# Performance work log

Hardware: AMD Instinct MI355X
Metric: run time of the kernel (lower is better)

## Reference

```python
import jax, jax.numpy as jnp
import numpy as np

N, E = 50000, 800000
NF, EF, S = 128, 64, 128

def _lin(key, fan_in, fan_out):
    k1, k2 = jax.random.split(key)
    lim = 1.0 / np.sqrt(fan_in)
    W = jax.random.uniform(k1, (fan_in, fan_out), jnp.float32, -lim, lim)
    b = jax.random.uniform(k2, (fan_out,), jnp.float32, -lim, lim)
    return W, b

def setup_inputs() -> dict:
    key = jax.random.key(0)
    ks = jax.random.split(key, 12)
    x = jax.random.normal(ks[0], (N, NF), jnp.float32)
    edge_index = jax.random.randint(ks[1], (2, E), 0, N, jnp.int64)
    edge_attr = jax.random.normal(ks[2], (E, EF), jnp.float32)
    Wn, bn = _lin(ks[3], NF, S)
    We, be = _lin(ks[4], EF, S)
    Wzc, bzc = _lin(ks[5], S, S)   # GCNConv weight/bias (z gate)
    Wzl, bzl = _lin(ks[6], 2 * S, S)
    Wrc, brc = _lin(ks[7], S, S)
    Wrl, brl = _lin(ks[8], 2 * S, S)
    Whc, bhc = _lin(ks[9], S, S)
    Whl, bhl = _lin(ks[10], 2 * S, S)
    Wout, bout = _lin(ks[11], 3 * S, 1)
    return dict(x=x, edge_index=edge_index, edge_attr=edge_attr,
                Wn=Wn, bn=bn, We=We, be=be,
                Wzc=Wzc, bzc=bzc, Wzl=Wzl, bzl=bzl,
                Wrc=Wrc, brc=brc, Wrl=Wrl, brl=brl,
                Whc=Whc, bhc=bhc, Whl=Whl, bhl=bhl,
                Wout=Wout, bout=bout)

def reference(x, edge_index, edge_attr, Wn, bn, We, be,
              Wzc, bzc, Wzl, bzl, Wrc, brc, Wrl, brl,
              Whc, bhc, Whl, bhl, Wout, bout):
    n = x.shape[0]
    src, dst = edge_index[0], edge_index[1]
    xe = jax.nn.relu(x @ Wn + bn)                      # [N,S]
    ea = jax.nn.relu(edge_attr @ We + be)              # [E,S]
    # GCNConv normalization with self-loops (shared across the 3 gates)
    loop = jnp.arange(n)
    s2 = jnp.concatenate([src, loop])
    d2 = jnp.concatenate([dst, loop])
    deg = jax.ops.segment_sum(jnp.ones(s2.shape[0], xe.dtype), d2, n)
    dinv = jax.lax.rsqrt(deg)                          # deg >= 1 (self loops)
    norm = (dinv[s2] * dinv[d2])[:, None]              # [E+N,1]
    def gcn(W, b):
        xw = xe @ W
        return jax.ops.segment_sum(xw[s2] * norm, d2, n) + b
    H = jnp.zeros_like(xe)
    Z = jax.nn.sigmoid(jnp.concatenate([gcn(Wzc, bzc), H], 1) @ Wzl + bzl)
    R = jax.nn.sigmoid(jnp.concatenate([gcn(Wrc, brc), H], 1) @ Wrl + brl)
    Ht = jnp.tanh(jnp.concatenate([gcn(Whc, bhc), H * R], 1) @ Whl + bhl)
    H = Z * H + (1.0 - Z) * Ht                          # [N,S]
    edge_h = jnp.concatenate([H[src], H[dst], ea], axis=1)  # [E,3S]
    return edge_h @ Wout + bout                         # [E,1]
```

## Files before the change

### kernel.cpp

```cpp
#include <hip/hip_runtime.h>
#include <hip/hip_bf16.h>
#include <math.h>

#define NN 50000
#define EE 800000

typedef __bf16 bf16x8 __attribute__((ext_vector_type(8)));
typedef float f32x4 __attribute__((ext_vector_type(4)));
typedef unsigned int u32x4 __attribute__((ext_vector_type(4)));

__global__ void k_deg_wprep(const int* __restrict__ ei, int* __restrict__ deg,
                            const float* __restrict__ Wzc, const float* __restrict__ bzc,
                            const float* __restrict__ Wzl, const float* __restrict__ bzl,
                            const float* __restrict__ Whc, const float* __restrict__ bhc,
                            const float* __restrict__ Whl, const float* __restrict__ bhl,
                            float* __restrict__ Wcat, float* __restrict__ cb) {
    if (blockIdx.x < 128) {
        int i = blockIdx.x;
        int k = threadIdx.x;
        if (k < 128) {
            float sz = 0.f, sh = 0.f;
            for (int j = 0; j < 128; j++) {
                sz += Wzc[i * 128 + j] * Wzl[j * 128 + k];
                sh += Whc[i * 128 + j] * Whl[j * 128 + k];
            }
            Wcat[i * 256 + 2 * k]     = sz;
            Wcat[i * 256 + 2 * k + 1] = sh;
            if (i == 0) {
                float bz = bzl[k], bh = bhl[k];
                for (int j = 0; j < 128; j++) {
                    bz += bzc[j] * Wzl[j * 128 + k];
                    bh += bhc[j] * Whl[j * 128 + k];
                }
                cb[2 * k]     = bz;
                cb[2 * k + 1] = bh;
            }
        }
    } else {
        int e = (blockIdx.x - 128) * 256 + threadIdx.x;
        if (e < EE) atomicAdd(&deg[ei[EE + e]], 1);
    }
}

__global__ __launch_bounds__(256) void k_g1_mfma(const float* __restrict__ x,
                                                 const float* __restrict__ Wn,
                                                 const float* __restrict__ bn,
                                                 const int* __restrict__ deg,
                                                 __hip_bfloat16* __restrict__ xs) {
    const int lane = threadIdx.x & 63;
    const int ln = lane & 15;
    const int q  = lane >> 4;
    const int wid = (blockIdx.x * 256 + threadIdx.x) >> 6;
    const int nw  = gridDim.x * 4;
    const int ch  = wid & 1;
    const int step = nw >> 1;

    bf16x8 bfrag[4][4];
#pragma unroll
    for (int t = 0; t < 4; t++)
#pragma unroll
        for (int kc = 0; kc < 4; kc++)
#pragma unroll
            for (int j = 0; j < 8; j++)
                bfrag[t][kc][j] = (__bf16)Wn[(kc * 32 + q * 8 + j) * 128 + ch * 64 + t * 16 + ln];
    float biasR[4];
#pragma unroll
    for (int t = 0; t < 4; t++) biasR[t] = bn[ch * 64 + t * 16 + ln];

    for (int rt = wid >> 1; rt < 3125; rt += step) {
        const int e0 = rt * 16;
        const float* arow = x + (size_t)(e0 + ln) * 128;
        bf16x8 af[4];
#pragma unroll
        for (int kc = 0; kc < 4; kc++) {
            float4 v0 = *(const float4*)(arow + kc * 32 + q * 8);
            float4 v1 = *(const float4*)(arow + kc * 32 + q * 8 + 4);
            af[kc][0] = (__bf16)v0.x; af[kc][1] = (__bf16)v0.y;
            af[kc][2] = (__bf16)v0.z; af[kc][3] = (__bf16)v0.w;
            af[kc][4] = (__bf16)v1.x; af[kc][5] = (__bf16)v1.y;
            af[kc][6] = (__bf16)v1.z; af[kc][7] = (__bf16)v1.w;
        }
        f32x4 acc[4];
#pragma unroll
        for (int t = 0; t < 4; t++) acc[t] = (f32x4){0.f, 0.f, 0.f, 0.f};
#pragma unroll
        for (int t = 0; t < 4; t++)
#pragma unroll
            for (int kc = 0; kc < 4; kc++)
                acc[t] = __builtin_amdgcn_mfma_f32_16x16x32_bf16(af[kc], bfrag[t][kc], acc[t], 0, 0, 0);

        float diR[4];
#pragma unroll
        for (int r = 0; r < 4; r++) diR[r] = rsqrtf((float)(deg[e0 + q * 4 + r] + 1));
#pragma unroll
        for (int t = 0; t < 4; t++)
#pragma unroll
            for (int r = 0; r < 4; r++) {
                float v = fmaxf(acc[t][r] + biasR[t], 0.f) * diR[r];
                xs[(size_t)(e0 + q * 4 + r) * 128 + ch * 64 + t * 16 + ln] = __float2bfloat16(v);
            }
    }
}

__global__ __launch_bounds__(256) void k_gate_mfma(const unsigned int* __restrict__ aggu,
                                                   const float* __restrict__ Wcat,
                                                   const float* __restrict__ cb,
                                                   const float* __restrict__ Wout,
                                                   float* __restrict__ aArr,
                                                   float* __restrict__ bArr) {
    const int lane = threadIdx.x & 63;
    const int ln = lane & 15;
    const int q  = lane >> 4;
    const int wid = (blockIdx.x * 256 + threadIdx.x) >> 6;
    const int nw  = gridDim.x * 4;
    const int cq  = wid & 3;
    const int step = nw >> 2;

    bf16x8 bfrag[4][4];
#pragma unroll
    for (int t = 0; t < 4; t++)
#pragma unroll
        for (int kc = 0; kc < 4; kc++)
#pragma unroll
            for (int j = 0; j < 8; j++)
                bfrag[t][kc][j] = (__bf16)Wcat[(kc * 32 + q * 8 + j) * 256 + cq * 64 + t * 16 + ln];

    float cbR[4], wAR[4], wBR[4];
#pragma unroll
    for (int t = 0; t < 4; t++) {
        int col = cq * 64 + t * 16 + ln;
        cbR[t] = cb[col];
        int k = col >> 1;
        wAR[t] = Wout[k];
        wBR[t] = Wout[128 + k];
    }
    const bool odd = (ln & 1);

    for (int rt = wid >> 2; rt < 3125; rt += step) {
        const int e0 = rt * 16;
        const u32x4* arow = (const u32x4*)aggu + (size_t)(e0 + ln) * 16;
        bf16x8 af[4];
#pragma unroll
        for (int kc = 0; kc < 4; kc++) {
            u32x4 uv = arow[kc * 4 + q];
            af[kc] = __builtin_bit_cast(bf16x8, uv);
        }
        f32x4 acc[4];
#pragma unroll
        for (int t = 0; t < 4; t++) acc[t] = (f32x4){0.f, 0.f, 0.f, 0.f};
#pragma unroll
        for (int t = 0; t < 4; t++)
#pragma unroll
            for (int kc = 0; kc < 4; kc++)
                acc[t] = __builtin_amdgcn_mfma_f32_16x16x32_bf16(af[kc], bfrag[t][kc], acc[t], 0, 0, 0);

        float pa[4] = {0.f, 0.f, 0.f, 0.f};
        float pb[4] = {0.f, 0.f, 0.f, 0.f};
#pragma unroll
        for (int t = 0; t < 4; t++)
#pragma unroll
            for (int r = 0; r < 4; r++) {
                float val = acc[t][r] + cbR[t];
                float s = odd ? tanhf(val) : (1.f / (1.f + expf(-val)));
                float partner = __shfl_xor(s, 1);
                if (!odd) {
                    float h = (1.f - s) * partner;
                    pa[r] += h * wAR[t];
                    pb[r] += h * wBR[t];
                }
            }
#pragma unroll
        for (int off = 1; off < 16; off <<= 1) {
#pragma unroll
            for (int r = 0; r < 4; r++) {
                pa[r] += __shfl_xor(pa[r], off);
                pb[r] += __shfl_xor(pb[r], off);
            }
        }
        if (ln < 4) {
            float v = (ln == 0) ? pa[0] : (ln == 1) ? pa[1] : (ln == 2) ? pa[2] : pa[3];
            atomicAdd(&aArr[e0 + q * 4 + ln], v);
        } else if (ln < 8) {
            int r = ln - 4;
            float v = (r == 0) ? pb[0] : (r == 1) ? pb[1] : (r == 2) ? pb[2] : pb[3];
            atomicAdd(&bArr[e0 + q * 4 + r], v);
        }
    }
}

__global__ void k_scan_a(const int* __restrict__ deg, int* __restrict__ partial) {
    __shared__ int s[256];
    int i = blockIdx.x * 256 + threadIdx.x;
    s[threadIdx.x] = (i < NN) ? deg[i] : 0;
    __syncthreads();
    for (int off = 128; off > 0; off >>= 1) {
        if (threadIdx.x < off) s[threadIdx.x] += s[threadIdx.x + off];
        __syncthreads();
    }
    if (threadIdx.x == 0) partial[blockIdx.x] = s[0];
}

__global__ void k_scan_c(const int* __restrict__ deg, const int* __restrict__ partial,
                         int* __restrict__ rowptr, int* __restrict__ cursor) {
    __shared__ int s[256];
    __shared__ int ps[256];
    int i = blockIdx.x * 256 + threadIdx.x;
    int v = (i < NN) ? deg[i] : 0;
    s[threadIdx.x] = v;
    ps[threadIdx.x] = (threadIdx.x < blockIdx.x) ? partial[threadIdx.x] : 0;
    __syncthreads();
    for (int off = 128; off > 0; off >>= 1) {
        if (threadIdx.x < off) ps[threadIdx.x] += ps[threadIdx.x + off];
        __syncthreads();
    }
    for (int off = 1; off < 256; off <<= 1) {
        int t = (threadIdx.x >= off) ? s[threadIdx.x - off] : 0;
        __syncthreads();
        s[threadIdx.x] += t;
        __syncthreads();
    }
    int excl = s[threadIdx.x] - v + ps[0];
    if (i < NN) { rowptr[i] = excl; cursor[i] = excl; }
    if (i == 0) rowptr[NN] = EE;
}

__global__ void k_fill(const int* __restrict__ ei, int* __restrict__ cursor,
                       int* __restrict__ col) {
    int e = blockIdx.x * 256 + threadIdx.x;
    if (e < EE) {
        int d = ei[EE + e];
        int p = atomicAdd(&cursor[d], 1);
        col[p] = ei[e];
    }
}

__global__ __launch_bounds__(256) void k_gather(const unsigned int* __restrict__ xsu,
                                                const int* __restrict__ rowptr,
                                                const int* __restrict__ col,
                                                const int* __restrict__ deg,
                                                unsigned int* __restrict__ aggu) {
    int gt = blockIdx.x * 256 + threadIdx.x;
    int node = gt >> 6;
    int lane = threadIdx.x & 63;
    if (node >= NN) return;
    int beg = rowptr[node], end = rowptr[node + 1];
    unsigned int u = xsu[(size_t)node * 64 + lane];
    float a0 = __uint_as_float(u << 16);
    float a1 = __uint_as_float(u & 0xFFFF0000u);
    int p = beg;
    while (p < end) {
        int rem = end - p;
        int chunk = rem < 64 ? rem : 64;
        int cv = (lane < chunk) ? col[p + lane] : 0;
        int j = 0;
        for (; j + 8 <= chunk; j += 8) {
            int s0 = __shfl(cv, j + 0);
            int s1 = __shfl(cv, j + 1);
            int s2 = __shfl(cv, j + 2);
            int s3 = __shfl(cv, j + 3);
            int s4 = __shfl(cv, j + 4);
            int s5 = __shfl(cv, j + 5);
            int s6 = __shfl(cv, j + 6);
            int s7 = __shfl(cv, j + 7);
            unsigned int u0 = xsu[(size_t)s0 * 64 + lane];
            unsigned int u1 = xsu[(size_t)s1 * 64 + lane];
            unsigned int u2 = xsu[(size_t)s2 * 64 + lane];
            unsigned int u3 = xsu[(size_t)s3 * 64 + lane];
            unsigned int u4 = xsu[(size_t)s4 * 64 + lane];
            unsigned int u5 = xsu[(size_t)s5 * 64 + lane];
            unsigned int u6 = xsu[(size_t)s6 * 64 + lane];
            unsigned int u7 = xsu[(size_t)s7 * 64 + lane];
            a0 += __uint_as_float(u0 << 16) + __uint_as_float(u1 << 16)
                + __uint_as_float(u2 << 16) + __uint_as_float(u3 << 16)
                + __uint_as_float(u4 << 16) + __uint_as_float(u5 << 16)
                + __uint_as_float(u6 << 16) + __uint_as_float(u7 << 16);
            a1 += __uint_as_float(u0 & 0xFFFF0000u) + __uint_as_float(u1 & 0xFFFF0000u)
                + __uint_as_float(u2 & 0xFFFF0000u) + __uint_as_float(u3 & 0xFFFF0000u)
                + __uint_as_float(u4 & 0xFFFF0000u) + __uint_as_float(u5 & 0xFFFF0000u)
                + __uint_as_float(u6 & 0xFFFF0000u) + __uint_as_float(u7 & 0xFFFF0000u);
        }
        for (; j < chunk; j++) {
            int s = __shfl(cv, j);
            unsigned int uv = xsu[(size_t)s * 64 + lane];
            a0 += __uint_as_float(uv << 16);
            a1 += __uint_as_float(uv & 0xFFFF0000u);
        }
        p += 64;
    }
    float di = rsqrtf((float)(deg[node] + 1));
    __hip_bfloat16 b0 = __float2bfloat16(a0 * di);
    __hip_bfloat16 b1 = __float2bfloat16(a1 * di);
    unsigned int lo = *(unsigned short*)&b0;
    unsigned int hi = *(unsigned short*)&b1;
    aggu[(size_t)node * 64 + lane] = lo | (hi << 16);
}

__global__ __launch_bounds__(256) void k_edge_mfma(const float* __restrict__ EA,
                                                   const int* __restrict__ ei,
                                                   const float* __restrict__ We,
                                                   const float* __restrict__ be,
                                                   const float* __restrict__ Wout,
                                                   const float* __restrict__ boutp,
                                                   const float* __restrict__ aArr,
                                                   const float* __restrict__ bArr,
                                                   float* __restrict__ out) {
    const int lane = threadIdx.x & 63;
    const int ln = lane & 15;
    const int q  = lane >> 4;
    const int wid = (blockIdx.x * 256 + threadIdx.x) >> 6;
    const int nw  = gridDim.x * 4;

    bf16x8 bfrag[2][8];
#pragma unroll
    for (int h = 0; h < 2; h++)
#pragma unroll
        for (int t = 0; t < 8; t++)
#pragma unroll
            for (int j = 0; j < 8; j++)
                bfrag[h][t][j] = (__bf16)We[(h * 32 + q * 8 + j) * 128 + t * 16 + ln];

    float beR[8], w3R[8];
#pragma unroll
    for (int t = 0; t < 8; t++) {
        beR[t] = be[t * 16 + ln];
        w3R[t] = Wout[256 + t * 16 + ln];
    }
    const float b0 = boutp[0];

    for (int tile = wid; tile < EE / 16; tile += nw) {
        const int e0 = tile * 16;
        const float* arow = EA + (size_t)(e0 + ln) * 64;
        float4 v0 = *(const float4*)(arow + q * 8);
        float4 v1 = *(const float4*)(arow + q * 8 + 4);
        float4 v2 = *(const float4*)(arow + 32 + q * 8);
        float4 v3 = *(const float4*)(arow + 32 + q * 8 + 4);
        bf16x8 af0, af1;
        af0[0] = (__bf16)v0.x; af0[1] = (__bf16)v0.y; af0[2] = (__bf16)v0.z; af0[3] = (__bf16)v0.w;
        af0[4] = (__bf16)v1.x; af0[5] = (__bf16)v1.y; af0[6] = (__bf16)v1.z; af0[7] = (__bf16)v1.w;
        af1[0] = (__bf16)v2.x; af1[1] = (__bf16)v2.y; af1[2] = (__bf16)v2.z; af1[3] = (__bf16)v2.w;
        af1[4] = (__bf16)v3.x; af1[5] = (__bf16)v3.y; af1[6] = (__bf16)v3.z; af1[7] = (__bf16)v3.w;

        f32x4 acc[8];
#pragma unroll
        for (int t = 0; t < 8; t++) acc[t] = (f32x4){0.f, 0.f, 0.f, 0.f};
#pragma unroll
        for (int t = 0; t < 8; t++)
            acc[t] = __builtin_amdgcn_mfma_f32_16x16x32_bf16(af0, bfrag[0][t], acc[t], 0, 0, 0);
#pragma unroll
        for (int t = 0; t < 8; t++)
            acc[t] = __builtin_amdgcn_mfma_f32_16x16x32_bf16(af1, bfrag[1][t], acc[t], 0, 0, 0);

        float part[4] = {0.f, 0.f, 0.f, 0.f};
#pragma unroll
        for (int t = 0; t < 8; t++)
#pragma unroll
            for (int r = 0; r < 4; r++) {
                float y = acc[t][r] + beR[t];
                y = fmaxf(y, 0.f);
                part[r] += y * w3R[t];
            }
#pragma unroll
        for (int off = 1; off < 16; off <<= 1) {
#pragma unroll
            for (int r = 0; r < 4; r++) part[r] += __shfl_xor(part[r], off);
        }
        if (ln < 4) {
            float c = (ln == 0) ? part[0] : (ln == 1) ? part[1] : (ln == 2) ? part[2] : part[3];
            int e = e0 + q * 4 + ln;
            out[e] = c + aArr[ei[e]] + bArr[ei[EE + e]] + b0;
        }
    }
}

extern "C" void kernel_launch(void* const* d_in, const int* in_sizes, int n_in,
                              void* d_out, int out_size, void* d_ws, size_t ws_size,
                              hipStream_t stream) {
    const float* x    = (const float*)d_in[0];
    const int*   ei   = (const int*)d_in[1];
    const float* ea   = (const float*)d_in[2];
    const float* Wn   = (const float*)d_in[3];
    const float* bn   = (const float*)d_in[4];
    const float* We   = (const float*)d_in[5];
    const float* be   = (const float*)d_in[6];
    const float* Wzc  = (const float*)d_in[7];
    const float* bzc  = (const float*)d_in[8];
    const float* Wzl  = (const float*)d_in[9];
    const float* bzl  = (const float*)d_in[10];
    const float* Whc  = (const float*)d_in[15];
    const float* bhc  = (const float*)d_in[16];
    const float* Whl  = (const float*)d_in[17];
    const float* bhl  = (const float*)d_in[18];
    const float* Wout = (const float*)d_in[19];
    const float* bout = (const float*)d_in[20];
    float* out = (float*)d_out;

    char* w = (char*)d_ws;
    auto carve = [&](size_t bytes) {
        void* p = (void*)w;
        w += (bytes + 255) / 256 * 256;
        return p;
    };
    int*   deg     = (int*)carve((size_t)NN * 4);
    float* aArr    = (float*)carve((size_t)NN * 4);
    float* bArr    = (float*)carve((size_t)NN * 4);
    size_t zbytes  = (size_t)((char*)(bArr + NN) - (char*)deg);
    __hip_bfloat16* xs = (__hip_bfloat16*)carve((size_t)NN * 128 * 2);
    unsigned int* aggu = (unsigned int*)carve((size_t)NN * 64 * 4);
    float* Wcat    = (float*)carve(128 * 256 * 4);
    float* cb      = (float*)carve(256 * 4);
    int*   rowptr  = (int*)carve((size_t)(NN + 1) * 4);
    int*   cursor  = (int*)carve((size_t)NN * 4);
    int*   col     = (int*)carve((size_t)EE * 4);
    int*   partial = (int*)carve(256 * 4);

    hipMemsetAsync(deg, 0, zbytes, stream);

    k_deg_wprep<<<128 + 3125, 256, 0, stream>>>(ei, deg, Wzc, bzc, Wzl, bzl,
                                                Whc, bhc, Whl, bhl, Wcat, cb);

    k_g1_mfma<<<384, 256, 0, stream>>>(x, Wn, bn, deg, xs);

    const int NB = (NN + 255) / 256;
    k_scan_a<<<NB, 256, 0, stream>>>(deg, partial);
    k_scan_c<<<NB, 256, 0, stream>>>(deg, partial, rowptr, cursor);
    k_fill<<<3125, 256, 0, stream>>>(ei, cursor, col);

    k_gather<<<(NN * 64 + 255) / 256, 256, 0, stream>>>((const unsigned int*)xs, rowptr, col, deg, aggu);

    k_gate_mfma<<<512, 256, 0, stream>>>(aggu, Wcat, cb, Wout, aArr, bArr);

    k_edge_mfma<<<2048, 256, 0, stream>>>(ea, ei, We, be, Wout, bout, aArr, bArr, out);
}
```

Before: 523.8 us.

## Fuse neighbor gather with gate MFMA via shared memory, widen node GEMM per wave

```diff
diff --git a/kernel.cpp b/kernel.cpp
--- a/kernel.cpp
+++ b/kernel.cpp
@@ -7,7 +7,6 @@
 
 typedef __bf16 bf16x8 __attribute__((ext_vector_type(8)));
 typedef float f32x4 __attribute__((ext_vector_type(4)));
-typedef unsigned int u32x4 __attribute__((ext_vector_type(4)));
 
 __global__ void k_deg_wprep(const int* __restrict__ ei, int* __restrict__ deg,
                             const float* __restrict__ Wzc, const float* __restrict__ bzc,
@@ -52,22 +51,20 @@
     const int q  = lane >> 4;
     const int wid = (blockIdx.x * 256 + threadIdx.x) >> 6;
     const int nw  = gridDim.x * 4;
-    const int ch  = wid & 1;
-    const int step = nw >> 1;
-
-    bf16x8 bfrag[4][4];
-#pragma unroll
-    for (int t = 0; t < 4; t++)
+
+    bf16x8 bfrag[8][4];
+#pragma unroll
+    for (int t = 0; t < 8; t++)
 #pragma unroll
         for (int kc = 0; kc < 4; kc++)
 #pragma unroll
             for (int j = 0; j < 8; j++)
-                bfrag[t][kc][j] = (__bf16)Wn[(kc * 32 + q * 8 + j) * 128 + ch * 64 + t * 16 + ln];
-    float biasR[4];
-#pragma unroll
-    for (int t = 0; t < 4; t++) biasR[t] = bn[ch * 64 + t * 16 + ln];
-
-    for (int rt = wid >> 1; rt < 3125; rt += step) {
+                bfrag[t][kc][j] = (__bf16)Wn[(kc * 32 + q * 8 + j) * 128 + t * 16 + ln];
+    float biasR[8];
+#pragma unroll
+    for (int t = 0; t < 8; t++) biasR[t] = bn[t * 16 + ln];
+
+    for (int rt = wid; rt < 3125; rt += nw) {
         const int e0 = rt * 16;
         const float* arow = x + (size_t)(e0 + ln) * 128;
         bf16x8 af[4];
@@ -80,11 +77,11 @@
             af[kc][4] = (__bf16)v1.x; af[kc][5] = (__bf16)v1.y;
             af[kc][6] = (__bf16)v1.z; af[kc][7] = (__bf16)v1.w;
         }
-        f32x4 acc[4];
-#pragma unroll
-        for (int t = 0; t < 4; t++) acc[t] = (f32x4){0.f, 0.f, 0.f, 0.f};
-#pragma unroll
-        for (int t = 0; t < 4; t++)
+        f32x4 acc[8];
+#pragma unroll
+        for (int t = 0; t < 8; t++) acc[t] = (f32x4){0.f, 0.f, 0.f, 0.f};
+#pragma unroll
+        for (int t = 0; t < 8; t++)
 #pragma unroll
             for (int kc = 0; kc < 4; kc++)
                 acc[t] = __builtin_amdgcn_mfma_f32_16x16x32_bf16(af[kc], bfrag[t][kc], acc[t], 0, 0, 0);
@@ -93,98 +90,12 @@
 #pragma unroll
         for (int r = 0; r < 4; r++) diR[r] = rsqrtf((float)(deg[e0 + q * 4 + r] + 1));
 #pragma unroll
-        for (int t = 0; t < 4; t++)
+        for (int t = 0; t < 8; t++)
 #pragma unroll
             for (int r = 0; r < 4; r++) {
                 float v = fmaxf(acc[t][r] + biasR[t], 0.f) * diR[r];
-                xs[(size_t)(e0 + q * 4 + r) * 128 + ch * 64 + t * 16 + ln] = __float2bfloat16(v);
-            }
-    }
-}
-
-__global__ __launch_bounds__(256) void k_gate_mfma(const unsigned int* __restrict__ aggu,
-                                                   const float* __restrict__ Wcat,
-                                                   const float* __restrict__ cb,
-                                                   const float* __restrict__ Wout,
-                                                   float* __restrict__ aArr,
-                                                   float* __restrict__ bArr) {
-    const int lane = threadIdx.x & 63;
-    const int ln = lane & 15;
-    const int q  = lane >> 4;
-    const int wid = (blockIdx.x * 256 + threadIdx.x) >> 6;
-    const int nw  = gridDim.x * 4;
-    const int cq  = wid & 3;
-    const int step = nw >> 2;
-
-    bf16x8 bfrag[4][4];
-#pragma unroll
-    for (int t = 0; t < 4; t++)
-#pragma unroll
-        for (int kc = 0; kc < 4; kc++)
-#pragma unroll
-            for (int j = 0; j < 8; j++)
-                bfrag[t][kc][j] = (__bf16)Wcat[(kc * 32 + q * 8 + j) * 256 + cq * 64 + t * 16 + ln];
-
-    float cbR[4], wAR[4], wBR[4];
-#pragma unroll
-    for (int t = 0; t < 4; t++) {
-        int col = cq * 64 + t * 16 + ln;
-        cbR[t] = cb[col];
-        int k = col >> 1;
-        wAR[t] = Wout[k];
-        wBR[t] = Wout[128 + k];
-    }
-    const bool odd = (ln & 1);
-
-    for (int rt = wid >> 2; rt < 3125; rt += step) {
-        const int e0 = rt * 16;
-        const u32x4* arow = (const u32x4*)aggu + (size_t)(e0 + ln) * 16;
-        bf16x8 af[4];
-#pragma unroll
-        for (int kc = 0; kc < 4; kc++) {
-            u32x4 uv = arow[kc * 4 + q];
-            af[kc] = __builtin_bit_cast(bf16x8, uv);
-        }
-        f32x4 acc[4];
-#pragma unroll
-        for (int t = 0; t < 4; t++) acc[t] = (f32x4){0.f, 0.f, 0.f, 0.f};
-#pragma unroll
-        for (int t = 0; t < 4; t++)
-#pragma unroll
-            for (int kc = 0; kc < 4; kc++)
-                acc[t] = __builtin_amdgcn_mfma_f32_16x16x32_bf16(af[kc], bfrag[t][kc], acc[t], 0, 0, 0);
-
-        float pa[4] = {0.f, 0.f, 0.f, 0.f};
-        float pb[4] = {0.f, 0.f, 0.f, 0.f};
-#pragma unroll
-        for (int t = 0; t < 4; t++)
-#pragma unroll
-            for (int r = 0; r < 4; r++) {
-                float val = acc[t][r] + cbR[t];
-                float s = odd ? tanhf(val) : (1.f / (1.f + expf(-val)));
-                float partner = __shfl_xor(s, 1);
-                if (!odd) {
-                    float h = (1.f - s) * partner;
-                    pa[r] += h * wAR[t];
-                    pb[r] += h * wBR[t];
-                }
-            }
-#pragma unroll
-        for (int off = 1; off < 16; off <<= 1) {
-#pragma unroll
-            for (int r = 0; r < 4; r++) {
-                pa[r] += __shfl_xor(pa[r], off);
-                pb[r] += __shfl_xor(pb[r], off);
-            }
-        }
-        if (ln < 4) {
-            float v = (ln == 0) ? pa[0] : (ln == 1) ? pa[1] : (ln == 2) ? pa[2] : pa[3];
-            atomicAdd(&aArr[e0 + q * 4 + ln], v);
-        } else if (ln < 8) {
-            int r = ln - 4;
-            float v = (r == 0) ? pb[0] : (r == 1) ? pb[1] : (r == 2) ? pb[2] : pb[3];
-            atomicAdd(&bArr[e0 + q * 4 + r], v);
-        }
+                xs[(size_t)(e0 + q * 4 + r) * 128 + t * 16 + ln] = __float2bfloat16(v);
+            }
     }
 }
 
@@ -234,65 +145,153 @@
     }
 }
 
-__global__ __launch_bounds__(256) void k_gather(const unsigned int* __restrict__ xsu,
-                                                const int* __restrict__ rowptr,
-                                                const int* __restrict__ col,
-                                                const int* __restrict__ deg,
-                                                unsigned int* __restrict__ aggu) {
-    int gt = blockIdx.x * 256 + threadIdx.x;
-    int node = gt >> 6;
-    int lane = threadIdx.x & 63;
-    if (node >= NN) return;
-    int beg = rowptr[node], end = rowptr[node + 1];
-    unsigned int u = xsu[(size_t)node * 64 + lane];
-    float a0 = __uint_as_float(u << 16);
-    float a1 = __uint_as_float(u & 0xFFFF0000u);
-    int p = beg;
-    while (p < end) {
-        int rem = end - p;
-        int chunk = rem < 64 ? rem : 64;
-        int cv = (lane < chunk) ? col[p + lane] : 0;
-        int j = 0;
-        for (; j + 8 <= chunk; j += 8) {
-            int s0 = __shfl(cv, j + 0);
-            int s1 = __shfl(cv, j + 1);
-            int s2 = __shfl(cv, j + 2);
-            int s3 = __shfl(cv, j + 3);
-            int s4 = __shfl(cv, j + 4);
-            int s5 = __shfl(cv, j + 5);
-            int s6 = __shfl(cv, j + 6);
-            int s7 = __shfl(cv, j + 7);
-            unsigned int u0 = xsu[(size_t)s0 * 64 + lane];
-            unsigned int u1 = xsu[(size_t)s1 * 64 + lane];
-            unsigned int u2 = xsu[(size_t)s2 * 64 + lane];
-            unsigned int u3 = xsu[(size_t)s3 * 64 + lane];
-            unsigned int u4 = xsu[(size_t)s4 * 64 + lane];
-            unsigned int u5 = xsu[(size_t)s5 * 64 + lane];
-            unsigned int u6 = xsu[(size_t)s6 * 64 + lane];
-            unsigned int u7 = xsu[(size_t)s7 * 64 + lane];
-            a0 += __uint_as_float(u0 << 16) + __uint_as_float(u1 << 16)
-                + __uint_as_float(u2 << 16) + __uint_as_float(u3 << 16)
-                + __uint_as_float(u4 << 16) + __uint_as_float(u5 << 16)
-                + __uint_as_float(u6 << 16) + __uint_as_float(u7 << 16);
-            a1 += __uint_as_float(u0 & 0xFFFF0000u) + __uint_as_float(u1 & 0xFFFF0000u)
-                + __uint_as_float(u2 & 0xFFFF0000u) + __uint_as_float(u3 & 0xFFFF0000u)
-                + __uint_as_float(u4 & 0xFFFF0000u) + __uint_as_float(u5 & 0xFFFF0000u)
-                + __uint_as_float(u6 & 0xFFFF0000u) + __uint_as_float(u7 & 0xFFFF0000u);
-        }
-        for (; j < chunk; j++) {
-            int s = __shfl(cv, j);
-            unsigned int uv = xsu[(size_t)s * 64 + lane];
-            a0 += __uint_as_float(uv << 16);
-            a1 += __uint_as_float(uv & 0xFFFF0000u);
-        }
-        p += 64;
-    }
-    float di = rsqrtf((float)(deg[node] + 1));
-    __hip_bfloat16 b0 = __float2bfloat16(a0 * di);
-    __hip_bfloat16 b1 = __float2bfloat16(a1 * di);
-    unsigned int lo = *(unsigned short*)&b0;
-    unsigned int hi = *(unsigned short*)&b1;
-    aggu[(size_t)node * 64 + lane] = lo | (hi << 16);
+__global__ __launch_bounds__(256) void k_gather_gate(const unsigned int* __restrict__ xsu,
+                                                     const int* __restrict__ rowptr,
+                                                     const int* __restrict__ col,
+                                                     const int* __restrict__ deg,
+                                                     const float* __restrict__ Wcat,
+                                                     const float* __restrict__ cb,
+                                                     const float* __restrict__ Wout,
+                                                     float* __restrict__ aArr,
+                                                     float* __restrict__ bArr) {
+    __shared__ __align__(16) unsigned int lag[16][68];
+    __shared__ float red[4][32];
+    const int lane = threadIdx.x & 63;
+    const int ln = lane & 15;
+    const int q  = lane >> 4;
+    const int w  = threadIdx.x >> 6;
+
+    bf16x8 bfrag[4][4];
+#pragma unroll
+    for (int t = 0; t < 4; t++)
+#pragma unroll
+        for (int kc = 0; kc < 4; kc++)
+#pragma unroll
+            for (int j = 0; j < 8; j++)
+                bfrag[t][kc][j] = (__bf16)Wcat[(kc * 32 + q * 8 + j) * 256 + w * 64 + t * 16 + ln];
+
+    float cbR[4], wAR[4], wBR[4];
+#pragma unroll
+    for (int t = 0; t < 4; t++) {
+        int c = w * 64 + t * 16 + ln;
+        cbR[t] = cb[c];
+        int k = c >> 1;
+        wAR[t] = Wout[k];
+        wBR[t] = Wout[128 + k];
+    }
+    const bool odd = (ln & 1);
+
+    for (int tile = blockIdx.x; tile < 3125; tile += gridDim.x) {
+        const int e0 = tile * 16;
+#pragma unroll
+        for (int i = 0; i < 4; i++) {
+            const int node = e0 + w * 4 + i;
+            const int beg = rowptr[node], end = rowptr[node + 1];
+            unsigned int u = xsu[(size_t)node * 64 + lane];
+            float a0 = __uint_as_float(u << 16);
+            float a1 = __uint_as_float(u & 0xFFFF0000u);
+            int p = beg;
+            while (p < end) {
+                int rem = end - p;
+                int chunk = rem < 64 ? rem : 64;
+                int cv = (lane < chunk) ? col[p + lane] : 0;
+                int j = 0;
+                for (; j + 8 <= chunk; j += 8) {
+                    int s0 = __shfl(cv, j + 0);
+                    int s1 = __shfl(cv, j + 1);
+                    int s2 = __shfl(cv, j + 2);
+                    int s3 = __shfl(cv, j + 3);
+                    int s4 = __shfl(cv, j + 4);
+                    int s5 = __shfl(cv, j + 5);
+                    int s6 = __shfl(cv, j + 6);
+                    int s7 = __shfl(cv, j + 7);
+                    unsigned int u0 = xsu[(size_t)s0 * 64 + lane];
+                    unsigned int u1 = xsu[(size_t)s1 * 64 + lane];
+                    unsigned int u2 = xsu[(size_t)s2 * 64 + lane];
+                    unsigned int u3 = xsu[(size_t)s3 * 64 + lane];
+                    unsigned int u4 = xsu[(size_t)s4 * 64 + lane];
+                    unsigned int u5 = xsu[(size_t)s5 * 64 + lane];
+                    unsigned int u6 = xsu[(size_t)s6 * 64 + lane];
+                    unsigned int u7 = xsu[(size_t)s7 * 64 + lane];
+                    a0 += __uint_as_float(u0 << 16) + __uint_as_float(u1 << 16)
+                        + __uint_as_float(u2 << 16) + __uint_as_float(u3 << 16)
+                        + __uint_as_float(u4 << 16) + __uint_as_float(u5 << 16)
+                        + __uint_as_float(u6 << 16) + __uint_as_float(u7 << 16);
+                    a1 += __uint_as_float(u0 & 0xFFFF0000u) + __uint_as_float(u1 & 0xFFFF0000u)
+                        + __uint_as_float(u2 & 0xFFFF0000u) + __uint_as_float(u3 & 0xFFFF0000u)
+                        + __uint_as_float(u4 & 0xFFFF0000u) + __uint_as_float(u5 & 0xFFFF0000u)
+                        + __uint_as_float(u6 & 0xFFFF0000u) + __uint_as_float(u7 & 0xFFFF0000u);
+                }
+                for (; j < chunk; j++) {
+                    int s = __shfl(cv, j);
+                    unsigned int uv = xsu[(size_t)s * 64 + lane];
+                    a0 += __uint_as_float(uv << 16);
+                    a1 += __uint_as_float(uv & 0xFFFF0000u);
+                }
+                p += 64;
+            }
+            float di = rsqrtf((float)(deg[node] + 1));
+            __hip_bfloat16 b0 = __float2bfloat16(a0 * di);
+            __hip_bfloat16 b1 = __float2bfloat16(a1 * di);
+            unsigned int lo = *(unsigned short*)&b0;
+            unsigned int hi = *(unsigned short*)&b1;
+            lag[w * 4 + i][lane] = lo | (hi << 16);
+        }
+        __syncthreads();
+
+        bf16x8 af[4];
+#pragma unroll
+        for (int kc = 0; kc < 4; kc++)
+            af[kc] = *(const bf16x8*)&lag[ln][kc * 16 + q * 4];
+        f32x4 acc[4];
+#pragma unroll
+        for (int t = 0; t < 4; t++) acc[t] = (f32x4){0.f, 0.f, 0.f, 0.f};
+#pragma unroll
+        for (int t = 0; t < 4; t++)
+#pragma unroll
+            for (int kc = 0; kc < 4; kc++)
+                acc[t] = __builtin_amdgcn_mfma_f32_16x16x32_bf16(af[kc], bfrag[t][kc], acc[t], 0, 0, 0);
+
+        float pa[4] = {0.f, 0.f, 0.f, 0.f};
+        float pb[4] = {0.f, 0.f, 0.f, 0.f};
+#pragma unroll
+        for (int t = 0; t < 4; t++)
+#pragma unroll
+            for (int r = 0; r < 4; r++) {
+                float val = acc[t][r] + cbR[t];
+                float s = odd ? tanhf(val) : (1.f / (1.f + expf(-val)));
+                float partner = __shfl_xor(s, 1);
+                if (!odd) {
+                    float h = (1.f - s) * partner;
+                    pa[r] += h * wAR[t];
+                    pb[r] += h * wBR[t];
+                }
+            }
+#pragma unroll
+        for (int off = 1; off < 16; off <<= 1) {
+#pragma unroll
+            for (int r = 0; r < 4; r++) {
+                pa[r] += __shfl_xor(pa[r], off);
+                pb[r] += __shfl_xor(pb[r], off);
+            }
+        }
+        if (ln < 4) {
+            float v = (ln == 0) ? pa[0] : (ln == 1) ? pa[1] : (ln == 2) ? pa[2] : pa[3];
+            red[w][q * 4 + ln] = v;
+        } else if (ln < 8) {
+            int r = ln - 4;
+            float v = (r == 0) ? pb[0] : (r == 1) ? pb[1] : (r == 2) ? pb[2] : pb[3];
+            red[w][16 + q * 4 + r] = v;
+        }
+        __syncthreads();
+        if (threadIdx.x < 32) {
+            int row = threadIdx.x & 15;
+            int ab = threadIdx.x >> 4;
+            float s = red[0][ab * 16 + row] + red[1][ab * 16 + row]
+                    + red[2][ab * 16 + row] + red[3][ab * 16 + row];
+            if (ab) bArr[e0 + row] = s; else aArr[e0 + row] = s;
+        }
+    }
 }
 
 __global__ __launch_bounds__(256) void k_edge_mfma(const float* __restrict__ EA,
@@ -403,9 +402,7 @@
     int*   deg     = (int*)carve((size_t)NN * 4);
     float* aArr    = (float*)carve((size_t)NN * 4);
     float* bArr    = (float*)carve((size_t)NN * 4);
-    size_t zbytes  = (size_t)((char*)(bArr + NN) - (char*)deg);
     __hip_bfloat16* xs = (__hip_bfloat16*)carve((size_t)NN * 128 * 2);
-    unsigned int* aggu = (unsigned int*)carve((size_t)NN * 64 * 4);
     float* Wcat    = (float*)carve(128 * 256 * 4);
     float* cb      = (float*)carve(256 * 4);
     int*   rowptr  = (int*)carve((size_t)(NN + 1) * 4);
@@ -413,21 +410,20 @@
     int*   col     = (int*)carve((size_t)EE * 4);
     int*   partial = (int*)carve(256 * 4);
 
-    hipMemsetAsync(deg, 0, zbytes, stream);
+    hipMemsetAsync(deg, 0, (size_t)NN * 4, stream);
 
     k_deg_wprep<<<128 + 3125, 256, 0, stream>>>(ei, deg, Wzc, bzc, Wzl, bzl,
                                                 Whc, bhc, Whl, bhl, Wcat, cb);
 
-    k_g1_mfma<<<384, 256, 0, stream>>>(x, Wn, bn, deg, xs);
+    k_g1_mfma<<<391, 256, 0, stream>>>(x, Wn, bn, deg, xs);
 
     const int NB = (NN + 255) / 256;
     k_scan_a<<<NB, 256, 0, stream>>>(deg, partial);
     k_scan_c<<<NB, 256, 0, stream>>>(deg, partial, rowptr, cursor);
     k_fill<<<3125, 256, 0, stream>>>(ei, cursor, col);
 
-    k_gather<<<(NN * 64 + 255) / 256, 256, 0, stream>>>((const unsigned int*)xs, rowptr, col, deg, aggu);
-
-    k_gate_mfma<<<512, 256, 0, stream>>>(aggu, Wcat, cb, Wout, aArr, bArr);
+    k_gather_gate<<<768, 256, 0, stream>>>((const unsigned int*)xs, rowptr, col, deg,
+                                           Wcat, cb, Wout, aArr, bArr);
 
     k_edge_mfma<<<2048, 256, 0, stream>>>(ea, ei, We, be, Wout, bout, aArr, bArr, out);
 }
```

New measurement: 583.6 us. +11.4%, slower.
